# Performance work log

Hardware: AMD Instinct MI355X
Metric: run time of the kernel (lower is better)

The kernel has to match this reference:

```python
import jax, jax.numpy as jnp
from jax import lax
import numpy as np

IN, H, OUT, G = 1, 32, 30, 4 * 32  # input_size, hidden_size, output_size, gate dim


def _lstm_layer(x_tbd, Wih, Whh, bih, bhh):
    # x_tbd: [T, B, D_in]; torch gate order: i, f, g, o
    B = x_tbd.shape[1]
    h0 = jnp.zeros((B, H), x_tbd.dtype)
    c0 = jnp.zeros((B, H), x_tbd.dtype)

    def step(carry, xt):
        h, c = carry
        z = xt @ Wih.T + h @ Whh.T + (bih + bhh)  # [B, 4H]
        i, f, g, o = jnp.split(z, 4, axis=-1)
        c = jax.nn.sigmoid(f) * c + jax.nn.sigmoid(i) * jnp.tanh(g)
        h = jax.nn.sigmoid(o) * jnp.tanh(c)
        return (h, c), h

    (hT, cT), hs = lax.scan(step, (h0, c0), x_tbd)
    return hs, hT


def setup_inputs() -> dict:
    key = jax.random.key(0)
    ks = jax.random.split(key, 16)
    B, T = 4096, 512
    s = 1.0 / np.sqrt(H)  # torch LSTM init scale
    inp = {"x": jax.random.normal(ks[0], (B, T, IN), dtype=jnp.float32)}
    for l, din in enumerate([IN, H, H]):
        inp[f"Wih{l}"] = jax.random.uniform(ks[1 + 4 * l], (G, din), jnp.float32, -s, s)
        inp[f"Whh{l}"] = jax.random.uniform(ks[2 + 4 * l], (G, H), jnp.float32, -s, s)
        inp[f"bih{l}"] = jax.random.uniform(ks[3 + 4 * l], (G,), jnp.float32, -s, s)
        inp[f"bhh{l}"] = jax.random.uniform(ks[4 + 4 * l], (G,), jnp.float32, -s, s)
    inp["W2"] = jax.random.uniform(ks[13], (OUT, H), jnp.float32, -s, s)
    inp["b2"] = jax.random.uniform(ks[14], (OUT,), jnp.float32, -s, s)
    return inp


def reference(x, Wih0, Whh0, bih0, bhh0, Wih1, Whh1, bih1, bhh1,
              Wih2, Whh2, bih2, bhh2, W2, b2):
    # batch_first input -> time-major for scan
    xt = jnp.transpose(x, (1, 0, 2))  # [T, B, IN]
    hs, _ = _lstm_layer(xt, Wih0, Whh0, bih0, bhh0)
    hs, _ = _lstm_layer(hs, Wih1, Whh1, bih1, bhh1)
    _, h_last = _lstm_layer(hs, Wih2, Whh2, bih2, bhh2)  # h[-1]: [B, H]
    return h_last @ W2.T + b2  # [B, OUT]
```

## Files before the change

### kernel.cpp

```cpp
#include <hip/hip_runtime.h>
#include <cstdint>
#include <cstddef>

#define TT   512
#define MT   16
#define OUTN 30

typedef __attribute__((ext_vector_type(8))) short short8;
typedef __attribute__((ext_vector_type(4))) float floatx4;

#define NLOG2E  (-1.4426950408889634f)
#define N2LOG2E (-2.8853900817779268f)

static __device__ __forceinline__ float rcpf(float x) { return __builtin_amdgcn_rcpf(x); }
static __device__ __forceinline__ float ex2(float x)  { return __builtin_amdgcn_exp2f(x); }

static __device__ __forceinline__ unsigned short cvt_bf16(float f) {
    unsigned int r;
    asm("v_cvt_pk_bf16_f32 %0, %1, %2" : "=v"(r) : "v"(f), "v"(f));
    return (unsigned short)r;
}
static __device__ __forceinline__ unsigned short to_bf16(float f) {
    union { float f; unsigned int u; } v; v.f = f;
    return (unsigned short)((v.u + 0x7FFFu + ((v.u >> 16) & 1u)) >> 16);
}

static __device__ __forceinline__ float gate_scale(int gate) {
    return (gate == 2) ? N2LOG2E : NLOG2E;
}

static __device__ __forceinline__ short8 load_frag_perm(const float* __restrict__ W, int arow, int k0) {
    int gate = arow & 3;
    int orig = gate * 32 + (arow >> 2);
    float s = gate_scale(gate);
    const float* p = W + orig * 32 + k0;
    short8 v;
#pragma unroll
    for (int e = 0; e < 8; ++e) v[e] = (short)to_bf16(s * p[e]);
    return v;
}
static __device__ __forceinline__ short8 load_frag_plain(const float* __restrict__ W, int row, int k0) {
    const float* p = W + row * 32 + k0;
    short8 v;
#pragma unroll
    for (int e = 0; e < 8; ++e) v[e] = (short)to_bf16(p[e]);
    return v;
}

static __device__ __forceinline__ unsigned short lstm_gates(floatx4 z, float& c) {
    float Di = 1.0f + ex2(z[0]);
    float Df = 1.0f + ex2(z[1]);
    float Dg = 1.0f + ex2(z[2]);
    float Do = 1.0f + ex2(z[3]);
    float rif = rcpf(Di * Df);
    float i = Df * rif;
    float f = Di * rif;
    float rgo = rcpf(Dg * Do);
    float g = __builtin_fmaf(2.0f, Do * rgo, -1.0f);
    float o = Dg * rgo;
    c = __builtin_fmaf(f, c, i * g);
    float tc = rcpf(1.0f + ex2(N2LOG2E * c));
    float h = __builtin_fmaf(o + o, tc, -o);
    return cvt_bf16(h);
}

__global__ __launch_bounds__(512, 2) void lstm_fused(
    const float* __restrict__ x,
    const float* __restrict__ Wih0, const float* __restrict__ Whh0,
    const float* __restrict__ bih0, const float* __restrict__ bhh0,
    const float* __restrict__ Wih1, const float* __restrict__ Whh1,
    const float* __restrict__ bih1, const float* __restrict__ bhh1,
    const float* __restrict__ Wih2, const float* __restrict__ Whh2,
    const float* __restrict__ bih2, const float* __restrict__ bhh2,
    const float* __restrict__ W2,   const float* __restrict__ b2,
    float* __restrict__ out)
{
    __shared__ float xs[MT][TT + 4];
    __shared__ unsigned short h0s[2][4][MT][8];
    __shared__ unsigned short h1s[2][4][MT][8];
    __shared__ unsigned short h2s[2][4][MT][8];

    const int tid  = (int)threadIdx.x;
    const int wv   = tid >> 6;
    const int l    = tid & 63;
    const int b    = l & 15;
    const int q    = l >> 4;
    const int u    = 4 * wv + q;
    const int uc   = u >> 3, ue = u & 7;
    const int bt   = (int)blockIdx.x;
    const int arow = 16 * wv + b;
    const int k0   = q * 8;

    {
        const floatx4* xg = (const floatx4*)(x + (size_t)bt * MT * TT);
#pragma unroll
        for (int j = 0; j < 4; ++j) {
            int idx = tid + j * 512;
            int row = idx >> 7;
            int c4  = idx & 127;
            *(floatx4*)&xs[row][c4 * 4] = xg[idx];
        }
    }

    short8 whh0f = load_frag_perm(Whh0, arow, k0);
    short8 wih1f = load_frag_perm(Wih1, arow, k0);
    short8 whh1f = load_frag_perm(Whh1, arow, k0);
    short8 wih2f = load_frag_perm(Wih2, arow, k0);
    short8 whh2f = load_frag_perm(Whh2, arow, k0);

    float wx0[4];
    floatx4 bc0, bc1, bc2;
#pragma unroll
    for (int r = 0; r < 4; ++r) {
        int idx = r * 32 + u;
        float s = gate_scale(r);
        wx0[r] = s * Wih0[idx];
        bc0[r] = s * (bih0[idx] + bhh0[idx]);
        bc1[r] = s * (bih1[idx] + bhh1[idx]);
        bc2[r] = s * (bih2[idx] + bhh2[idx]);
    }

    short8 w2f = {};
    floatx4 b2c = {0.f, 0.f, 0.f, 0.f};
    if (wv < 2) {
        int r2 = 16 * wv + b;
        int rc = r2 < OUTN ? r2 : OUTN - 1;
        w2f = load_frag_plain(W2, rc, k0);
#pragma unroll
        for (int r = 0; r < 4; ++r) {
            int rr = 16 * wv + 4 * q + r;
            b2c[r] = (rr < OUTN) ? b2[rr] : 0.0f;
        }
    }

    float c0 = 0.f, c1 = 0.f, c2 = 0.f;

    __syncthreads();

    auto bc0x = [&](float xv) {
        floatx4 c4v;
#pragma unroll
        for (int r = 0; r < 4; ++r) c4v[r] = __builtin_fmaf(xv, wx0[r], bc0[r]);
        return c4v;
    };

    {
        floatx4 z0 = bc0x(xs[b][0]);
        h0s[0][uc][b][ue] = lstm_gates(z0, c0);
        __syncthreads();
    }
    {
        short8 bh0 = *(const short8*)&h0s[0][q][b][0];
        floatx4 z0 = __builtin_amdgcn_mfma_f32_16x16x32_bf16(whh0f, bh0, bc0x(xs[b][1]), 0, 0, 0);
        floatx4 z1 = __builtin_amdgcn_mfma_f32_16x16x32_bf16(wih1f, bh0, bc1, 0, 0, 0);
        unsigned short h0b = lstm_gates(z0, c0);
        unsigned short h1b = lstm_gates(z1, c1);
        h0s[1][uc][b][ue] = h0b;
        h1s[1][uc][b][ue] = h1b;
        __syncthreads();
    }
    {
        short8 bh0 = *(const short8*)&h0s[1][q][b][0];
        short8 bh1 = *(const short8*)&h1s[1][q][b][0];
        floatx4 z0 = __builtin_amdgcn_mfma_f32_16x16x32_bf16(whh0f, bh0, bc0x(xs[b][2]), 0, 0, 0);
        floatx4 z1 = __builtin_amdgcn_mfma_f32_16x16x32_bf16(whh1f, bh1, bc1, 0, 0, 0);
        z1 = __builtin_amdgcn_mfma_f32_16x16x32_bf16(wih1f, bh0, z1, 0, 0, 0);
        floatx4 z2 = __builtin_amdgcn_mfma_f32_16x16x32_bf16(wih2f, bh1, bc2, 0, 0, 0);
        unsigned short h0b = lstm_gates(z0, c0);
        unsigned short h1b = lstm_gates(z1, c1);
        unsigned short h2b = lstm_gates(z2, c2);
        h0s[0][uc][b][ue] = h0b;
        h1s[0][uc][b][ue] = h1b;
        h2s[0][uc][b][ue] = h2b;
        __syncthreads();
    }

    auto STEP = [&](float xv, int wb) {
        const int rb = wb ^ 1;
        short8 bh0 = *(const short8*)&h0s[rb][q][b][0];
        short8 bh1 = *(const short8*)&h1s[rb][q][b][0];
        short8 bh2 = *(const short8*)&h2s[rb][q][b][0];
        floatx4 z0 = __builtin_amdgcn_mfma_f32_16x16x32_bf16(whh0f, bh0, bc0x(xv), 0, 0, 0);
        floatx4 z1 = __builtin_amdgcn_mfma_f32_16x16x32_bf16(whh1f, bh1, bc1, 0, 0, 0);
        floatx4 z2 = __builtin_amdgcn_mfma_f32_16x16x32_bf16(whh2f, bh2, bc2, 0, 0, 0);
        z1 = __builtin_amdgcn_mfma_f32_16x16x32_bf16(wih1f, bh0, z1, 0, 0, 0);
        z2 = __builtin_amdgcn_mfma_f32_16x16x32_bf16(wih2f, bh1, z2, 0, 0, 0);
        unsigned short h0b = lstm_gates(z0, c0);
        unsigned short h1b = lstm_gates(z1, c1);
        unsigned short h2b = lstm_gates(z2, c2);
        h0s[wb][uc][b][ue] = h0b;
        h1s[wb][uc][b][ue] = h1b;
        h2s[wb][uc][b][ue] = h2b;
        __syncthreads();
    };

    STEP(xs[b][3], 1);

    for (int k = 4; k < TT; k += 4) {
        floatx4 xq = *(const floatx4*)&xs[b][k];
        STEP(xq[0], 0);
        STEP(xq[1], 1);
        STEP(xq[2], 0);
        STEP(xq[3], 1);
    }

    {
        short8 bh0 = *(const short8*)&h0s[1][q][b][0];
        short8 bh1 = *(const short8*)&h1s[1][q][b][0];
        short8 bh2 = *(const short8*)&h2s[1][q][b][0];
        floatx4 z1 = __builtin_amdgcn_mfma_f32_16x16x32_bf16(whh1f, bh1, bc1, 0, 0, 0);
        z1 = __builtin_amdgcn_mfma_f32_16x16x32_bf16(wih1f, bh0, z1, 0, 0, 0);
        floatx4 z2 = __builtin_amdgcn_mfma_f32_16x16x32_bf16(whh2f, bh2, bc2, 0, 0, 0);
        z2 = __builtin_amdgcn_mfma_f32_16x16x32_bf16(wih2f, bh1, z2, 0, 0, 0);
        unsigned short h1b = lstm_gates(z1, c1);
        unsigned short h2b = lstm_gates(z2, c2);
        h1s[0][uc][b][ue] = h1b;
        h2s[0][uc][b][ue] = h2b;
        __syncthreads();
    }
    {
        short8 bh1 = *(const short8*)&h1s[0][q][b][0];
        short8 bh2 = *(const short8*)&h2s[0][q][b][0];
        floatx4 z2 = __builtin_amdgcn_mfma_f32_16x16x32_bf16(whh2f, bh2, bc2, 0, 0, 0);
        z2 = __builtin_amdgcn_mfma_f32_16x16x32_bf16(wih2f, bh1, z2, 0, 0, 0);
        h2s[1][uc][b][ue] = lstm_gates(z2, c2);
        __syncthreads();
    }

    if (wv < 2) {
        short8 bh2 = *(const short8*)&h2s[1][q][b][0];
        floatx4 zo = __builtin_amdgcn_mfma_f32_16x16x32_bf16(w2f, bh2, b2c, 0, 0, 0);
#pragma unroll
        for (int r = 0; r < 4; ++r) {
            int rr = 16 * wv + 4 * q + r;
            if (rr < OUTN)
                out[(size_t)(bt * MT + b) * OUTN + rr] = zo[r];
        }
    }
}

extern "C" void kernel_launch(void* const* d_in, const int* in_sizes, int n_in,
                              void* d_out, int out_size, void* d_ws, size_t ws_size,
                              hipStream_t stream) {
    const float* x    = (const float*)d_in[0];
    const float* Wih0 = (const float*)d_in[1];
    const float* Whh0 = (const float*)d_in[2];
    const float* bih0 = (const float*)d_in[3];
    const float* bhh0 = (const float*)d_in[4];
    const float* Wih1 = (const float*)d_in[5];
    const float* Whh1 = (const float*)d_in[6];
    const float* bih1 = (const float*)d_in[7];
    const float* bhh1 = (const float*)d_in[8];
    const float* Wih2 = (const float*)d_in[9];
    const float* Whh2 = (const float*)d_in[10];
    const float* bih2 = (const float*)d_in[11];
    const float* bhh2 = (const float*)d_in[12];
    const float* W2   = (const float*)d_in[13];
    const float* b2   = (const float*)d_in[14];
    float* out = (float*)d_out;

    dim3 grid(4096 / MT);
    dim3 block(512);
    hipLaunchKernelGGL(lstm_fused, grid, block, 0, stream,
                       x, Wih0, Whh0, bih0, bhh0,
                       Wih1, Whh1, bih1, bhh1,
                       Wih2, Whh2, bih2, bhh2, W2, b2, out);
}
```

Baseline: 255.7 us.

## Split LSTM layers across wave groups in 1024-thread blocks

Doubles the block to 16 waves. Waves 0-7 compute layers 0 and 1 through a new interleaved two-cell gate routine, and waves 8-15 compute layer 2, so each wave carries fewer MFMAs and fewer transcendental ops per timestep. The per-step critical path per wave gets shorter, but barriers now span 1024 threads. Launch bounds drop to one block per CU, which may reduce latency hiding across blocks.

```diff
diff --git a/kernel.cpp b/kernel.cpp
--- a/kernel.cpp
+++ b/kernel.cpp
@@ -64,7 +64,28 @@
     return cvt_bf16(h);
 }
 
-__global__ __launch_bounds__(512, 2) void lstm_fused(
+static __device__ __forceinline__ void gates2(floatx4 z0, floatx4 z1,
+                                              float& c0, float& c1,
+                                              unsigned short& h0b, unsigned short& h1b) {
+    float e00 = ex2(z0[0]), e01 = ex2(z0[1]), e02 = ex2(z0[2]), e03 = ex2(z0[3]);
+    float e10 = ex2(z1[0]), e11 = ex2(z1[1]), e12 = ex2(z1[2]), e13 = ex2(z1[3]);
+    float Di0 = 1.0f + e00, Df0 = 1.0f + e01, Dg0 = 1.0f + e02, Do0 = 1.0f + e03;
+    float Di1 = 1.0f + e10, Df1 = 1.0f + e11, Dg1 = 1.0f + e12, Do1 = 1.0f + e13;
+    float rif0 = rcpf(Di0 * Df0), rgo0 = rcpf(Dg0 * Do0);
+    float rif1 = rcpf(Di1 * Df1), rgo1 = rcpf(Dg1 * Do1);
+    float i0 = Df0 * rif0, f0 = Di0 * rif0, o0 = Dg0 * rgo0;
+    float i1 = Df1 * rif1, f1 = Di1 * rif1, o1 = Dg1 * rgo1;
+    float g0 = __builtin_fmaf(2.0f, Do0 * rgo0, -1.0f);
+    float g1 = __builtin_fmaf(2.0f, Do1 * rgo1, -1.0f);
+    c0 = __builtin_fmaf(f0, c0, i0 * g0);
+    c1 = __builtin_fmaf(f1, c1, i1 * g1);
+    float a0 = ex2(N2LOG2E * c0), a1 = ex2(N2LOG2E * c1);
+    float t0 = rcpf(1.0f + a0), t1 = rcpf(1.0f + a1);
+    h0b = cvt_bf16(__builtin_fmaf(o0 + o0, t0, -o0));
+    h1b = cvt_bf16(__builtin_fmaf(o1 + o1, t1, -o1));
+}
+
+__global__ __launch_bounds__(1024, 1) void lstm_fused(
     const float* __restrict__ x,
     const float* __restrict__ Wih0, const float* __restrict__ Whh0,
     const float* __restrict__ bih0, const float* __restrict__ bhh0,
@@ -85,39 +106,49 @@
     const int l    = tid & 63;
     const int b    = l & 15;
     const int q    = l >> 4;
-    const int u    = 4 * wv + q;
+    const bool aw  = (wv < 8);
+    const int wj   = aw ? wv : (wv - 8);
+    const int u    = 4 * wj + q;
     const int uc   = u >> 3, ue = u & 7;
     const int bt   = (int)blockIdx.x;
-    const int arow = 16 * wv + b;
+    const int arow = 16 * wj + b;
     const int k0   = q * 8;
 
     {
         const floatx4* xg = (const floatx4*)(x + (size_t)bt * MT * TT);
 #pragma unroll
-        for (int j = 0; j < 4; ++j) {
-            int idx = tid + j * 512;
+        for (int j = 0; j < 2; ++j) {
+            int idx = tid + j * 1024;
             int row = idx >> 7;
             int c4  = idx & 127;
             *(floatx4*)&xs[row][c4 * 4] = xg[idx];
         }
     }
 
-    short8 whh0f = load_frag_perm(Whh0, arow, k0);
-    short8 wih1f = load_frag_perm(Wih1, arow, k0);
-    short8 whh1f = load_frag_perm(Whh1, arow, k0);
-    short8 wih2f = load_frag_perm(Wih2, arow, k0);
-    short8 whh2f = load_frag_perm(Whh2, arow, k0);
-
-    float wx0[4];
-    floatx4 bc0, bc1, bc2;
-#pragma unroll
-    for (int r = 0; r < 4; ++r) {
-        int idx = r * 32 + u;
-        float s = gate_scale(r);
-        wx0[r] = s * Wih0[idx];
-        bc0[r] = s * (bih0[idx] + bhh0[idx]);
-        bc1[r] = s * (bih1[idx] + bhh1[idx]);
-        bc2[r] = s * (bih2[idx] + bhh2[idx]);
+    short8 whh0f = {}, wih1f = {}, whh1f = {}, wih2f = {}, whh2f = {};
+    float wx0[4] = {0.f, 0.f, 0.f, 0.f};
+    floatx4 bc0 = {0.f, 0.f, 0.f, 0.f}, bc1 = bc0, bc2 = bc0;
+    if (aw) {
+        whh0f = load_frag_perm(Whh0, arow, k0);
+        wih1f = load_frag_perm(Wih1, arow, k0);
+        whh1f = load_frag_perm(Whh1, arow, k0);
+#pragma unroll
+        for (int r = 0; r < 4; ++r) {
+            int idx = r * 32 + u;
+            float s = gate_scale(r);
+            wx0[r] = s * Wih0[idx];
+            bc0[r] = s * (bih0[idx] + bhh0[idx]);
+            bc1[r] = s * (bih1[idx] + bhh1[idx]);
+        }
+    } else {
+        wih2f = load_frag_perm(Wih2, arow, k0);
+        whh2f = load_frag_perm(Whh2, arow, k0);
+#pragma unroll
+        for (int r = 0; r < 4; ++r) {
+            int idx = r * 32 + u;
+            float s = gate_scale(r);
+            bc2[r] = s * (bih2[idx] + bhh2[idx]);
+        }
     }
 
     short8 w2f = {};
@@ -144,88 +175,93 @@
         return c4v;
     };
 
-    {
+    if (aw) {
         floatx4 z0 = bc0x(xs[b][0]);
         h0s[0][uc][b][ue] = lstm_gates(z0, c0);
-        __syncthreads();
-    }
-    {
+    }
+    __syncthreads();
+    if (aw) {
         short8 bh0 = *(const short8*)&h0s[0][q][b][0];
         floatx4 z0 = __builtin_amdgcn_mfma_f32_16x16x32_bf16(whh0f, bh0, bc0x(xs[b][1]), 0, 0, 0);
         floatx4 z1 = __builtin_amdgcn_mfma_f32_16x16x32_bf16(wih1f, bh0, bc1, 0, 0, 0);
-        unsigned short h0b = lstm_gates(z0, c0);
-        unsigned short h1b = lstm_gates(z1, c1);
+        unsigned short h0b, h1b;
+        gates2(z0, z1, c0, c1, h0b, h1b);
         h0s[1][uc][b][ue] = h0b;
         h1s[1][uc][b][ue] = h1b;
-        __syncthreads();
-    }
-    {
+    }
+    __syncthreads();
+    if (aw) {
         short8 bh0 = *(const short8*)&h0s[1][q][b][0];
         short8 bh1 = *(const short8*)&h1s[1][q][b][0];
         floatx4 z0 = __builtin_amdgcn_mfma_f32_16x16x32_bf16(whh0f, bh0, bc0x(xs[b][2]), 0, 0, 0);
         floatx4 z1 = __builtin_amdgcn_mfma_f32_16x16x32_bf16(whh1f, bh1, bc1, 0, 0, 0);
         z1 = __builtin_amdgcn_mfma_f32_16x16x32_bf16(wih1f, bh0, z1, 0, 0, 0);
-        floatx4 z2 = __builtin_amdgcn_mfma_f32_16x16x32_bf16(wih2f, bh1, bc2, 0, 0, 0);
-        unsigned short h0b = lstm_gates(z0, c0);
-        unsigned short h1b = lstm_gates(z1, c1);
-        unsigned short h2b = lstm_gates(z2, c2);
+        unsigned short h0b, h1b;
+        gates2(z0, z1, c0, c1, h0b, h1b);
         h0s[0][uc][b][ue] = h0b;
         h1s[0][uc][b][ue] = h1b;
-        h2s[0][uc][b][ue] = h2b;
-        __syncthreads();
-    }
+    } else {
+        short8 bh1 = *(const short8*)&h1s[1][q][b][0];
+        floatx4 z2 = __builtin_amdgcn_mfma_f32_16x16x32_bf16(wih2f, bh1, bc2, 0, 0, 0);
+        h2s[0][uc][b][ue] = lstm_gates(z2, c2);
+    }
+    __syncthreads();
 
     auto STEP = [&](float xv, int wb) {
         const int rb = wb ^ 1;
-        short8 bh0 = *(const short8*)&h0s[rb][q][b][0];
-        short8 bh1 = *(const short8*)&h1s[rb][q][b][0];
-        short8 bh2 = *(const short8*)&h2s[rb][q][b][0];
-        floatx4 z0 = __builtin_amdgcn_mfma_f32_16x16x32_bf16(whh0f, bh0, bc0x(xv), 0, 0, 0);
-        floatx4 z1 = __builtin_amdgcn_mfma_f32_16x16x32_bf16(whh1f, bh1, bc1, 0, 0, 0);
-        floatx4 z2 = __builtin_amdgcn_mfma_f32_16x16x32_bf16(whh2f, bh2, bc2, 0, 0, 0);
-        z1 = __builtin_amdgcn_mfma_f32_16x16x32_bf16(wih1f, bh0, z1, 0, 0, 0);
-        z2 = __builtin_amdgcn_mfma_f32_16x16x32_bf16(wih2f, bh1, z2, 0, 0, 0);
-        unsigned short h0b = lstm_gates(z0, c0);
-        unsigned short h1b = lstm_gates(z1, c1);
-        unsigned short h2b = lstm_gates(z2, c2);
-        h0s[wb][uc][b][ue] = h0b;
-        h1s[wb][uc][b][ue] = h1b;
-        h2s[wb][uc][b][ue] = h2b;
+        if (aw) {
+            short8 bh0 = *(const short8*)&h0s[rb][q][b][0];
+            short8 bh1 = *(const short8*)&h1s[rb][q][b][0];
+            floatx4 z0 = __builtin_amdgcn_mfma_f32_16x16x32_bf16(whh0f, bh0, bc0x(xv), 0, 0, 0);
+            floatx4 z1 = __builtin_amdgcn_mfma_f32_16x16x32_bf16(whh1f, bh1, bc1, 0, 0, 0);
+            z1 = __builtin_amdgcn_mfma_f32_16x16x32_bf16(wih1f, bh0, z1, 0, 0, 0);
+            unsigned short h0b, h1b;
+            gates2(z0, z1, c0, c1, h0b, h1b);
+            h0s[wb][uc][b][ue] = h0b;
+            h1s[wb][uc][b][ue] = h1b;
+        } else {
+            short8 bh1 = *(const short8*)&h1s[rb][q][b][0];
+            short8 bh2 = *(const short8*)&h2s[rb][q][b][0];
+            floatx4 z2 = __builtin_amdgcn_mfma_f32_16x16x32_bf16(whh2f, bh2, bc2, 0, 0, 0);
+            z2 = __builtin_amdgcn_mfma_f32_16x16x32_bf16(wih2f, bh1, z2, 0, 0, 0);
+            h2s[wb][uc][b][ue] = lstm_gates(z2, c2);
+        }
         __syncthreads();
     };
 
-    STEP(xs[b][3], 1);
+    STEP(aw ? xs[b][3] : 0.0f, 1);
 
     for (int k = 4; k < TT; k += 4) {
-        floatx4 xq = *(const floatx4*)&xs[b][k];
+        floatx4 xq = {0.f, 0.f, 0.f, 0.f};
+        if (aw) xq = *(const floatx4*)&xs[b][k];
         STEP(xq[0], 0);
         STEP(xq[1], 1);
         STEP(xq[2], 0);
         STEP(xq[3], 1);
     }
 
-    {
+    if (aw) {
         short8 bh0 = *(const short8*)&h0s[1][q][b][0];
         short8 bh1 = *(const short8*)&h1s[1][q][b][0];
-        short8 bh2 = *(const short8*)&h2s[1][q][b][0];
         floatx4 z1 = __builtin_amdgcn_mfma_f32_16x16x32_bf16(whh1f, bh1, bc1, 0, 0, 0);
         z1 = __builtin_amdgcn_mfma_f32_16x16x32_bf16(wih1f, bh0, z1, 0, 0, 0);
+        h1s[0][uc][b][ue] = lstm_gates(z1, c1);
+    } else {
+        short8 bh1 = *(const short8*)&h1s[1][q][b][0];
+        short8 bh2 = *(const short8*)&h2s[1][q][b][0];
         floatx4 z2 = __builtin_amdgcn_mfma_f32_16x16x32_bf16(whh2f, bh2, bc2, 0, 0, 0);
         z2 = __builtin_amdgcn_mfma_f32_16x16x32_bf16(wih2f, bh1, z2, 0, 0, 0);
-        unsigned short h1b = lstm_gates(z1, c1);
-        unsigned short h2b = lstm_gates(z2, c2);
-        h1s[0][uc][b][ue] = h1b;
-        h2s[0][uc][b][ue] = h2b;
-        __syncthreads();
-    }
-    {
+        h2s[0][uc][b][ue] = lstm_gates(z2, c2);
+    }
+    __syncthreads();
+    if (!aw) {
         short8 bh1 = *(const short8*)&h1s[0][q][b][0];
         short8 bh2 = *(const short8*)&h2s[0][q][b][0];
         floatx4 z2 = __builtin_amdgcn_mfma_f32_16x16x32_bf16(whh2f, bh2, bc2, 0, 0, 0);
         z2 = __builtin_amdgcn_mfma_f32_16x16x32_bf16(wih2f, bh1, z2, 0, 0, 0);
         h2s[1][uc][b][ue] = lstm_gates(z2, c2);
-        __syncthreads();
-    }
+    }
+    __syncthreads();
 
     if (wv < 2) {
         short8 bh2 = *(const short8*)&h2s[1][q][b][0];
@@ -260,7 +296,7 @@
     float* out = (float*)d_out;
 
     dim3 grid(4096 / MT);
-    dim3 block(512);
+    dim3 block(1024);
     hipLaunchKernelGGL(lstm_fused, grid, block, 0, stream,
                        x, Wih0, Whh0, bih0, bhh0,
                        Wih1, Whh1, bih1, bhh1,
```

Measured after the change: 247.4 us. 1.03x faster.
